# Optimization experiments

Measured on AMD Instinct MI355X. Metric: run time of the kernel, lower is better.

Reference implementation:

```python
import jax, jax.numpy as jnp
import numpy as np
import math

B, TH, STEPS = 4, 120, 8
D_IN, D_MODEL, N_HEADS, N_LAYERS, D_FF = 32, 512, 8, 4, 2048
N_SUB = 5
D_HEAD = D_MODEL // N_HEADS
EPS = 1e-5


def _pos_encoding(T, d):
    pos = jnp.arange(T, dtype=jnp.float32)[:, None]
    div = jnp.exp(jnp.arange(0, d, 2, dtype=jnp.float32) * (-math.log(10000.0) / d))
    pe = jnp.zeros((T, d), dtype=jnp.float32)
    pe = pe.at[:, 0::2].set(jnp.sin(pos * div))
    pe = pe.at[:, 1::2].set(jnp.cos(pos * div))
    return pe


def setup_inputs() -> dict:
    key = jax.random.key(0)
    ks = jax.random.split(key, 16)
    s = 0.02
    n = lambda k, shp: jax.random.normal(k, shp, jnp.float32) * s
    return {
        "history": jax.random.normal(ks[0], (B, TH, D_IN), jnp.float32),
        "steps": STEPS,
        "W_emb": n(ks[1], (D_MODEL, D_IN)),
        "b_emb": jnp.zeros((D_MODEL,), jnp.float32),
        "Wq": n(ks[2], (N_LAYERS, D_MODEL, D_MODEL)),
        "Wk": n(ks[3], (N_LAYERS, D_MODEL, D_MODEL)),
        "Wv": n(ks[4], (N_LAYERS, D_MODEL, D_MODEL)),
        "Wo": n(ks[5], (N_LAYERS, D_MODEL, D_MODEL)),
        "ln1_g": jnp.ones((N_LAYERS, D_MODEL), jnp.float32),
        "ln1_b": jnp.zeros((N_LAYERS, D_MODEL), jnp.float32),
        "W1": n(ks[6], (N_LAYERS, D_FF, D_MODEL)),
        "b1": jnp.zeros((N_LAYERS, D_FF), jnp.float32),
        "W2": n(ks[7], (N_LAYERS, D_MODEL, D_FF)),
        "b2": jnp.zeros((N_LAYERS, D_MODEL), jnp.float32),
        "ln2_g": jnp.ones((N_LAYERS, D_MODEL), jnp.float32),
        "ln2_b": jnp.zeros((N_LAYERS, D_MODEL), jnp.float32),
        "Wr1": n(ks[8], (D_FF, 2 * D_MODEL)),
        "br1": jnp.zeros((D_FF,), jnp.float32),
        "Wr2": n(ks[9], (D_IN, D_FF)),
        "br2": jnp.zeros((D_IN,), jnp.float32),
    }


def _layernorm(x, g, b):
    mu = x.mean(-1, keepdims=True)
    var = ((x - mu) ** 2).mean(-1, keepdims=True)
    return (x - mu) / jnp.sqrt(var + EPS) * g + b


def reference(history, steps, W_emb, b_emb, Wq, Wk, Wv, Wo, ln1_g, ln1_b,
              W1, b1, W2, b2, ln2_g, ln2_b, Wr1, br1, Wr2, br2):
    total_len = TH + steps
    pe = _pos_encoding(total_len, D_MODEL)
    idx = jnp.arange(total_len)
    # NOTE: faithful to source: mask True where kv index > q index (equinox: True = attend)
    mask = idx[:, None] < idx[None, :]
    neg = jnp.finfo(jnp.float32).min
    scale = math.sqrt(D_MODEL)

    def transformer(buf):  # buf: [T, D_IN] -> [T, D_MODEL]
        h = (buf @ W_emb.T + b_emb) * scale + pe
        for l in range(N_LAYERS):
            q = (h @ Wq[l].T).reshape(total_len, N_HEADS, D_HEAD)
            k = (h @ Wk[l].T).reshape(total_len, N_HEADS, D_HEAD)
            v = (h @ Wv[l].T).reshape(total_len, N_HEADS, D_HEAD)
            logits = jnp.einsum("qhd,khd->hqk", q, k) / math.sqrt(D_HEAD)
            logits = jnp.where(mask[None], logits, neg)
            w = jax.nn.softmax(logits, axis=-1)
            attn = jnp.einsum("hqk,khd->qhd", w, v).reshape(total_len, D_MODEL)
            h = _layernorm(h + attn @ Wo[l].T, ln1_g[l], ln1_b[l])
            m = jax.nn.gelu(h @ W1[l].T + b1[l]) @ W2[l].T + b2[l]
            h = _layernorm(h + m, ln2_g[l], ln2_b[l])
        return h

    def refine(start_val, ctx):  # start_val: [D_IN], ctx: [D_MODEL]
        def body(i, cur):
            we = (W_emb @ cur + b_emb) * scale
            comb = jnp.concatenate([we, ctx])
            delta = Wr2 @ jax.nn.gelu(Wr1 @ comb + br1) + br2
            return cur + delta
        return jax.lax.fori_loop(0, N_SUB, body, start_val)

    def single(hist):  # [TH, D_IN] -> [steps, D_IN]
        buf = jnp.zeros((total_len, D_IN), jnp.float32).at[:TH].set(hist)

        def scan_fn(buf, step_idx):
            h = transformer(buf)  # full recompute each decode step (no KV cache)
            ptr = TH + step_idx
            next_val = refine(buf[ptr - 1], h[ptr - 1])
            return buf.at[ptr].set(next_val), next_val

        _, preds = jax.lax.scan(scan_fn, buf, jnp.arange(steps))
        return preds

    return jax.vmap(single)(history)
```

## Files before the change

kernel.cpp:

```cpp
#include <hip/hip_runtime.h>
#include <math.h>

namespace {
constexpr int NB = 4;
constexpr int SEQ = 128;
constexpr int TH_ = 120;
constexpr int NSTEP = 8;
constexpr int DMODEL = 512;
constexpr int NHEAD = 8;
constexpr int DHEAD = 64;
constexpr int DFFN = 2048;
constexpr int DIN = 32;
constexpr int MROWS = NB*SEQ;
constexpr float SCALE_EMB = 22.627416997969522f;
constexpr float LN_EPS = 1e-5f;
constexpr float NEGF = -3.4028234663852886e38f;
constexpr float PE_C = -0.017988946039015984f;
}

using short8 = __attribute__((ext_vector_type(8))) short;
using f32x4  = __attribute__((ext_vector_type(4))) float;

__device__ __forceinline__ float wave_sum(float v){
#pragma unroll
  for(int off=32;off;off>>=1) v += __shfl_xor(v,off,64);
  return v;
}
__device__ __forceinline__ float blk_sum(float v, float* scr){
  v = wave_sum(v);
  __syncthreads();
  if((threadIdx.x&63)==0) scr[threadIdx.x>>6]=v;
  __syncthreads();
  return scr[0]+scr[1]+scr[2]+scr[3];
}
__device__ __forceinline__ float gelu_t(float x){
  float t = 0.7978845608028654f*(x + 0.044715f*x*x*x);
  return 0.5f*x*(1.0f + tanhf(t));
}
__device__ __forceinline__ float pe_val(int t, int d){
  float div = expf((float)(d & ~1) * PE_C);
  float a = (float)t * div;
  return (d & 1) ? cosf(a) : sinf(a);
}
__device__ __forceinline__ unsigned short f2b(float f){
  union { float f; unsigned u; } c; c.f = f;
  unsigned u = c.u + 0x7FFFu + ((c.u>>16)&1u);
  return (unsigned short)(u>>16);
}
__device__ __forceinline__ short8 pack8(const float* f){
  short8 s;
#pragma unroll
  for(int i=0;i<8;i++) s[i] = (short)f2b(f[i]);
  return s;
}

__global__ __launch_bounds__(256) void conv_w(const float* __restrict__ Wq,
                                              const float* __restrict__ Wk,
                                              const float* __restrict__ Wv,
                                              const float* __restrict__ Wo,
                                              const float* __restrict__ W1,
                                              const float* __restrict__ W2,
                                              unsigned short* __restrict__ dst){
  size_t base = ((size_t)blockIdx.x*256 + threadIdx.x)*8;
  if(base >= 12582912u) return;
  const float* src; size_t off;
  if(base < 1048576u){ src=Wq; off=base; }
  else if(base < 2097152u){ src=Wk; off=base-1048576u; }
  else if(base < 3145728u){ src=Wv; off=base-2097152u; }
  else if(base < 4194304u){ src=Wo; off=base-3145728u; }
  else if(base < 8388608u){ src=W1; off=base-4194304u; }
  else { src=W2; off=base-8388608u; }
  float4 a = *(const float4*)(src+off);
  float4 b = *(const float4*)(src+off+4);
  float f[8] = {a.x,a.y,a.z,a.w,b.x,b.y,b.z,b.w};
  *(short8*)(dst + base) = pack8(f);
}

__global__ __launch_bounds__(256) void init_h0(const float* __restrict__ hist,
                                               const float* __restrict__ W_emb,
                                               const float* __restrict__ b_emb,
                                               float* __restrict__ h0,
                                               unsigned short* __restrict__ h0b){
  int bt = blockIdx.x;
  int b = bt >> 7, t = bt & 127;
  __shared__ float x[DIN];
  if(threadIdx.x < DIN)
    x[threadIdx.x] = (t < TH_) ? hist[((size_t)b*TH_ + t)*DIN + threadIdx.x] : 0.f;
  __syncthreads();
  for(int d = threadIdx.x; d < DMODEL; d += 256){
    float s = 0.f;
#pragma unroll 8
    for(int i=0;i<DIN;i++) s += W_emb[d*DIN+i]*x[i];
    float v = SCALE_EMB*(s + b_emb[d]) + pe_val(t,d);
    h0[(size_t)bt*DMODEL + d] = v;
    h0b[(size_t)bt*DMODEL + d] = f2b(v);
  }
}

__global__ __launch_bounds__(256) void init_misc(const float* __restrict__ Wr1,
                                                 const float* __restrict__ W_emb,
                                                 const float* __restrict__ b_emb,
                                                 const float* __restrict__ br1,
                                                 const float* __restrict__ hist,
                                                 float* __restrict__ M1,
                                                 float* __restrict__ cb1,
                                                 float* __restrict__ cur_x){
  __shared__ float row[DMODEL];
  int j0 = blockIdx.x*8;
  for(int jj=0;jj<8;jj++){
    int j = j0+jj;
    for(int k=threadIdx.x;k<DMODEL;k+=256) row[k] = Wr1[(size_t)j*1024 + k];
    __syncthreads();
    if(threadIdx.x < DIN){
      int i = threadIdx.x; float s = 0.f;
      for(int k=0;k<DMODEL;k++) s += row[k]*W_emb[k*DIN+i];
      M1[j*DIN+i] = SCALE_EMB*s;
    } else if(threadIdx.x == DIN){
      float s=0.f;
      for(int k=0;k<DMODEL;k++) s += row[k]*b_emb[k];
      cb1[j] = br1[j] + SCALE_EMB*s;
    }
    __syncthreads();
  }
  if(blockIdx.x==0 && threadIdx.x<NB*DIN){
    int b = threadIdx.x>>5, i = threadIdx.x&31;
    cur_x[b*DIN+i] = hist[((size_t)b*TH_ + (TH_-1))*DIN + i];
  }
}

__global__ __launch_bounds__(256) void lnpass(const float* __restrict__ X,
                                              const float* __restrict__ g,
                                              const float* __restrict__ bta,
                                              float* __restrict__ Y,
                                              unsigned short* __restrict__ Yb){
  int row = blockIdx.x*4 + (threadIdx.x>>6);
  int l = threadIdx.x&63;
  const float* xp = X + (size_t)row*DMODEL + l*8;
  float4 x0 = *(const float4*)xp;
  float4 x1 = *(const float4*)(xp+4);
  float f[8] = {x0.x,x0.y,x0.z,x0.w,x1.x,x1.y,x1.z,x1.w};
  float s = 0.f;
#pragma unroll
  for(int i=0;i<8;i++) s += f[i];
  s = wave_sum(s);
  float mu = s*(1.f/DMODEL);
  float v = 0.f;
#pragma unroll
  for(int i=0;i<8;i++){ float d0=f[i]-mu; v += d0*d0; }
  v = wave_sum(v);
  float rs = rsqrtf(v*(1.f/DMODEL) + LN_EPS);
#pragma unroll
  for(int i=0;i<8;i++){
    int c = l*8+i;
    f[i] = (f[i]-mu)*rs*g[c] + bta[c];
  }
  float* yp = Y + (size_t)row*DMODEL + l*8;
  *(float4*)yp     = make_float4(f[0],f[1],f[2],f[3]);
  *(float4*)(yp+4) = make_float4(f[4],f[5],f[6],f[7]);
  *(short8*)(Yb + (size_t)row*DMODEL + l*8) = pack8(f);
}

__global__ __launch_bounds__(256) void gemm_bf(
    const unsigned short* __restrict__ A16, int Ka,
    const unsigned short* __restrict__ Wa,
    const unsigned short* __restrict__ Wb,
    const unsigned short* __restrict__ Wc,
    const float* __restrict__ bias, const float* __restrict__ resid,
    float* __restrict__ Cf, unsigned short* __restrict__ Cb,
    int c_rs, int c_mode, int act)
{
  int n0 = blockIdx.x*128;
  int m0 = blockIdx.y*64;
  int tid = threadIdx.x, w = tid>>6, ln = tid&63;
  __shared__ __align__(16) unsigned short As[64][72];
  __shared__ __align__(16) unsigned short Bs[128][72];

  const unsigned short* Wsrc; int nrow0;
  if(c_mode==2){ int which = n0>>9; Wsrc = (which==0?Wa:(which==1?Wb:Wc)); nrow0 = n0&511; }
  else { Wsrc = Wa; nrow0 = n0; }

  f32x4 acc[4][2];
#pragma unroll
  for(int i=0;i<4;i++)
#pragma unroll
    for(int j=0;j<2;j++) acc[i][j] = (f32x4){0.f,0.f,0.f,0.f};

  int fr = ln&15, fq = (ln>>4)*8;
  int arow = tid>>2, akq = (tid&3)*16;
  int brow = tid>>1, bkq = (tid&1)*32;

  for(int k0=0;k0<Ka;k0+=64){
    const unsigned short* ap = A16 + (size_t)(m0+arow)*Ka + k0 + akq;
    short8 a0 = *(const short8*)ap;
    short8 a1 = *(const short8*)(ap+8);
    const unsigned short* bp = Wsrc + (size_t)(nrow0+brow)*Ka + k0 + bkq;
    short8 b0 = *(const short8*)bp;
    short8 b1 = *(const short8*)(bp+8);
    short8 b2 = *(const short8*)(bp+16);
    short8 b3 = *(const short8*)(bp+24);
    *(short8*)&As[arow][akq]   = a0;
    *(short8*)&As[arow][akq+8] = a1;
    *(short8*)&Bs[brow][bkq]    = b0;
    *(short8*)&Bs[brow][bkq+8]  = b1;
    *(short8*)&Bs[brow][bkq+16] = b2;
    *(short8*)&Bs[brow][bkq+24] = b3;
    __syncthreads();
    short8 af[4][2], bf[2][2];
#pragma unroll
    for(int kf=0;kf<2;kf++){
#pragma unroll
      for(int rt=0;rt<4;rt++) af[rt][kf] = *(const short8*)&As[rt*16 + fr][kf*32 + fq];
#pragma unroll
      for(int ct=0;ct<2;ct++) bf[ct][kf] = *(const short8*)&Bs[32*w + ct*16 + fr][kf*32 + fq];
    }
#pragma unroll
    for(int kf=0;kf<2;kf++)
#pragma unroll
      for(int rt=0;rt<4;rt++)
#pragma unroll
        for(int ct=0;ct<2;ct++)
          acc[rt][ct] = __builtin_amdgcn_mfma_f32_16x16x32_bf16(af[rt][kf], bf[ct][kf], acc[rt][ct], 0, 0, 0);
    __syncthreads();
  }

#pragma unroll
  for(int rt=0;rt<4;rt++){
#pragma unroll
    for(int ct=0;ct<2;ct++){
      int n = n0 + 32*w + ct*16 + fr;
#pragma unroll
      for(int r=0;r<4;r++){
        int row = m0 + rt*16 + (ln>>4)*4 + r;
        float v = acc[rt][ct][r];
        if(bias)  v += bias[n];
        if(resid) v += resid[(size_t)row*DMODEL + n];
        if(act==1) v = gelu_t(v);
        if(c_mode==0)      Cf[(size_t)row*c_rs + n] = v;
        else if(c_mode==1) Cb[(size_t)row*c_rs + n] = f2b(v);
        else {
          int which = n>>9, rem = n&511;
          int b = row>>7, t = row&127;
          Cf[(size_t)which*(MROWS*DMODEL) +
             ((size_t)(b*NHEAD + (rem>>6))*SEQ + t)*DHEAD + (rem&63)] = v;
        }
      }
    }
  }
}

__global__ __launch_bounds__(256) void attn_k(const float* __restrict__ qb,
                                              const float* __restrict__ kb,
                                              const float* __restrict__ vb,
                                              unsigned short* __restrict__ attb){
  int b = blockIdx.z, h = blockIdx.y;
  int r0 = blockIdx.x*32;
  const float* Kh = kb + (size_t)(b*NHEAD+h)*SEQ*DHEAD;
  const float* Vh = vb + (size_t)(b*NHEAD+h)*SEQ*DHEAD;
  const float* Qh = qb + (size_t)(b*NHEAD+h)*SEQ*DHEAD;
  __shared__ float kv[SEQ][DHEAD];
  __shared__ float wsm[32][132];
  __shared__ float qs[32][68];
  int tid = threadIdx.x;
  int d = tid&63, rr = tid>>6;

  for(int k=rr;k<SEQ;k+=4) kv[k][d ^ (k&60)] = Kh[k*DHEAD + d];
  for(int r=rr;r<32;r+=4)  qs[r][d] = Qh[(size_t)(r0+r)*DHEAD + d];
  __syncthreads();

  {
    int rp = tid>>4;
    int kg = tid&15;
    float acc[2][8];
#pragma unroll
    for(int i=0;i<2;i++)
#pragma unroll
      for(int kk=0;kk<8;kk++) acc[i][kk]=0.f;
#pragma unroll 4
    for(int d4=0;d4<16;d4++){
      float4 q0 = *(const float4*)&qs[2*rp][d4*4];
      float4 q1 = *(const float4*)&qs[2*rp+1][d4*4];
#pragma unroll
      for(int kk=0;kk<8;kk++){
        int k = 8*kg + kk;
        int off = (d4*4) ^ (k&60);
        float4 kv4 = *(const float4*)&kv[k][off];
        acc[0][kk] += q0.x*kv4.x + q0.y*kv4.y + q0.z*kv4.z + q0.w*kv4.w;
        acc[1][kk] += q1.x*kv4.x + q1.y*kv4.y + q1.z*kv4.z + q1.w*kv4.w;
      }
    }
#pragma unroll
    for(int i=0;i<2;i++){
      int t = r0 + 2*rp + i;
#pragma unroll
      for(int kk=0;kk<8;kk++){
        int k = 8*kg + kk;
        wsm[2*rp+i][k] = (k > t) ? acc[i][kk]*0.125f : NEGF;
      }
    }
  }
  __syncthreads();

  {
    int l2 = tid&63, wv = tid>>6;
    for(int r=wv;r<32;r+=4){
      float l0 = wsm[r][l2], l1 = wsm[r][l2+64];
      float m = fmaxf(l0,l1);
#pragma unroll
      for(int off=32;off;off>>=1) m = fmaxf(m, __shfl_xor(m,off,64));
      float e0 = expf(l0-m), e1 = expf(l1-m);
      float s = e0+e1;
      s = wave_sum(s);
      float inv = 1.f/s;
      wsm[r][l2] = e0*inv; wsm[r][l2+64] = e1*inv;
    }
  }
  __syncthreads();

  for(int k=rr;k<SEQ;k+=4) kv[k][d] = Vh[k*DHEAD + d];
  __syncthreads();

  {
    int dq = (tid&15)*4, rg = tid>>4;
    for(int r=rg;r<32;r+=16){
      float4 acc2 = make_float4(0.f,0.f,0.f,0.f);
      for(int k=0;k<SEQ;k++){
        float w0 = wsm[r][k];
        float4 v = *(const float4*)&kv[k][dq];
        acc2.x += w0*v.x; acc2.y += w0*v.y; acc2.z += w0*v.z; acc2.w += w0*v.w;
      }
      int row = b*SEQ + r0 + r;
      unsigned short* op = attb + (size_t)row*DMODEL + h*DHEAD + dq;
      op[0]=f2b(acc2.x); op[1]=f2b(acc2.y); op[2]=f2b(acc2.z); op[3]=f2b(acc2.w);
    }
  }
}

__global__ __launch_bounds__(256) void ctx_k(const float* __restrict__ r2,
                                             const float* __restrict__ g2,
                                             const float* __restrict__ b2,
                                             const float* __restrict__ Wr1,
                                             const float* __restrict__ cb1,
                                             float* __restrict__ ctxt, int ptr){
  int b = blockIdx.y; int j0 = blockIdx.x*128;
  __shared__ float raw[DMODEL], ctx[DMODEL], scr[4];
  int tid = threadIdx.x;
  const float* rp = r2 + (size_t)(b*SEQ + ptr-1)*DMODEL;
  for(int k=tid;k<DMODEL;k+=256) raw[k]=rp[k];
  __syncthreads();
  float s = 0.f;
  for(int k=tid;k<DMODEL;k+=256) s += raw[k];
  s = blk_sum(s, scr);
  float mu = s/(float)DMODEL;
  float v = 0.f;
  for(int k=tid;k<DMODEL;k+=256){ float d0 = raw[k]-mu; v += d0*d0; }
  v = blk_sum(v, scr);
  float rs = rsqrtf(v/(float)DMODEL + LN_EPS);
  for(int k=tid;k<DMODEL;k+=256) ctx[k] = (raw[k]-mu)*rs*g2[k] + b2[k];
  __syncthreads();
  int wv = tid>>6, l2 = tid&63;
  for(int jj=wv;jj<128;jj+=4){
    int j = j0+jj;
    const float* wp = Wr1 + (size_t)j*1024 + 512;
    float acc = 0.f;
#pragma unroll
    for(int q=0;q<8;q++){ int k = l2 + 64*q; acc += wp[k]*ctx[k]; }
    acc = wave_sum(acc);
    if(l2==0) ctxt[b*DFFN + j] = acc + cb1[j];
  }
}

__global__ __launch_bounds__(256) void refine_fin(const float* __restrict__ M1,
                                                  const float* __restrict__ ctxt,
                                                  const float* __restrict__ Wr2,
                                                  const float* __restrict__ br2,
                                                  float* __restrict__ cur_x,
                                                  const float* __restrict__ W_emb,
                                                  const float* __restrict__ b_emb,
                                                  float* __restrict__ out,
                                                  float* __restrict__ h0,
                                                  unsigned short* __restrict__ h0b,
                                                  int s, int ptr){
  int b = blockIdx.x, tid = threadIdx.x;
  __shared__ float cur[DIN], gs[DFFN], dscr[DIN];
  if(tid < DIN) cur[tid] = cur_x[b*DIN + tid];
  __syncthreads();
  for(int sub=0; sub<5; sub++){
    for(int jj=tid; jj<DFFN; jj+=256){
      float u = ctxt[b*DFFN + jj];
      const float* mp = M1 + (size_t)jj*DIN;
#pragma unroll
      for(int p=0;p<8;p++){
        float4 mv = *(const float4*)(mp + 4*p);
        u += mv.x*cur[4*p] + mv.y*cur[4*p+1] + mv.z*cur[4*p+2] + mv.w*cur[4*p+3];
      }
      gs[jj] = gelu_t(u);
    }
    __syncthreads();
    int w = tid>>6, l = tid&63;
#pragma unroll
    for(int q=0;q<8;q++){
      int i = w*8 + q;
      const float* wr = Wr2 + (size_t)i*DFFN;
      float a = 0.f;
#pragma unroll
      for(int p=0;p<8;p++){
        int j0 = p*256 + l*4;
        float4 wv = *(const float4*)(wr + j0);
        float4 gv = *(const float4*)&gs[j0];
        a += wv.x*gv.x + wv.y*gv.y + wv.z*gv.z + wv.w*gv.w;
      }
      a = wave_sum(a);
      if(l==0) dscr[i] = a;
    }
    __syncthreads();
    if(tid < DIN) cur[tid] += dscr[tid] + br2[tid];
    __syncthreads();
  }
  if(tid < DIN){
    out[(b*NSTEP + s)*DIN + tid] = cur[tid];
    cur_x[b*DIN + tid] = cur[tid];
  }
  __syncthreads();
  for(int d=tid; d<DMODEL; d+=256){
    float s2 = 0.f;
#pragma unroll 8
    for(int i=0;i<DIN;i++) s2 += W_emb[d*DIN+i]*cur[i];
    float v = SCALE_EMB*(s2 + b_emb[d]) + pe_val(ptr, d);
    size_t idx = (size_t)(b*SEQ + ptr)*DMODEL + d;
    h0[idx] = v;
    h0b[idx] = f2b(v);
  }
}

extern "C" void kernel_launch(void* const* d_in, const int* in_sizes, int n_in,
                              void* d_out, int out_size, void* d_ws, size_t ws_size,
                              hipStream_t stream) {
  (void)in_sizes; (void)n_in; (void)out_size; (void)ws_size;
  const float* hist = (const float*)d_in[0];
  const float* W_emb= (const float*)d_in[2];
  const float* b_emb= (const float*)d_in[3];
  const float* Wq   = (const float*)d_in[4];
  const float* Wk   = (const float*)d_in[5];
  const float* Wv   = (const float*)d_in[6];
  const float* Wo   = (const float*)d_in[7];
  const float* ln1g = (const float*)d_in[8];
  const float* ln1b = (const float*)d_in[9];
  const float* W1   = (const float*)d_in[10];
  const float* b1   = (const float*)d_in[11];
  const float* W2   = (const float*)d_in[12];
  const float* b2v  = (const float*)d_in[13];
  const float* ln2g = (const float*)d_in[14];
  const float* ln2b = (const float*)d_in[15];
  const float* Wr1  = (const float*)d_in[16];
  const float* br1  = (const float*)d_in[17];
  const float* Wr2  = (const float*)d_in[18];
  const float* br2  = (const float*)d_in[19];
  float* out = (float*)d_out;
  float* ws  = (float*)d_ws;

  const size_t BTD = (size_t)MROWS*DMODEL;
  const size_t BTDH = BTD/2;
  float* h0   = ws;
  unsigned short* h0b = (unsigned short*)(h0 + BTD);
  float* r2   = h0 + BTD + BTDH;
  float* hln  = r2 + BTD;
  float* hp   = hln + BTD;
  unsigned short* hpb = (unsigned short*)(hp + BTD);
  float* qb   = hp + BTD + BTDH;
  float* kb   = qb + BTD;
  float* vb   = kb + BTD;
  unsigned short* attb = (unsigned short*)(vb + BTD);
  unsigned short* hlnb = (unsigned short*)(vb + BTD + BTDH);
  unsigned short* fbuf16 = (unsigned short*)qb;
  float* r1   = qb;
  unsigned short* W16 = (unsigned short*)(qb + 4*BTD);
  float* after_w = qb + 4*BTD + 6291456;
  float* M1   = after_w;
  float* cb1  = M1 + (size_t)DFFN*DIN;
  float* ctxt = cb1 + DFFN;
  float* cur_x= ctxt + NB*DFFN;

  unsigned short* Wq16 = W16;
  unsigned short* Wk16 = W16 + 1048576;
  unsigned short* Wv16 = W16 + 2097152;
  unsigned short* Wo16 = W16 + 3145728;
  unsigned short* W116 = W16 + 4194304;
  unsigned short* W216 = W16 + 8388608;

  conv_w<<<dim3(6144),dim3(256),0,stream>>>(Wq,Wk,Wv,Wo,W1,W2,W16);
  init_h0<<<dim3(MROWS),dim3(256),0,stream>>>(hist,W_emb,b_emb,h0,h0b);
  init_misc<<<dim3(256),dim3(256),0,stream>>>(Wr1,W_emb,b_emb,br1,hist,M1,cb1,cur_x);

  for(int s=0;s<NSTEP;s++){
    int ptr = TH_ + s;
    for(int l=0;l<4;l++){
      if(l>0)
        lnpass<<<dim3(128),dim3(256),0,stream>>>(r2, ln2g+(l-1)*DMODEL, ln2b+(l-1)*DMODEL, hln, hlnb);
      const unsigned short* A16 = (l==0)? h0b : hlnb;
      const float* res1 = (l==0)? h0 : hln;

      gemm_bf<<<dim3(12,8),dim3(256),0,stream>>>(A16, DMODEL,
          Wq16 + (size_t)l*262144, Wk16 + (size_t)l*262144, Wv16 + (size_t)l*262144,
          nullptr, nullptr, qb, nullptr, 0, 2, 0);

      attn_k<<<dim3(4,NHEAD,NB),dim3(256),0,stream>>>(qb,kb,vb,attb);

      gemm_bf<<<dim3(4,8),dim3(256),0,stream>>>(attb, DMODEL,
          Wo16 + (size_t)l*262144, nullptr, nullptr,
          nullptr, res1, r1, nullptr, DMODEL, 0, 0);

      lnpass<<<dim3(128),dim3(256),0,stream>>>(r1, ln1g+l*DMODEL, ln1b+l*DMODEL, hp, hpb);

      gemm_bf<<<dim3(16,8),dim3(256),0,stream>>>(hpb, DMODEL,
          W116 + (size_t)l*1048576, nullptr, nullptr,
          b1 + l*DFFN, nullptr, nullptr, fbuf16, DFFN, 1, 1);

      gemm_bf<<<dim3(4,8),dim3(256),0,stream>>>(fbuf16, DFFN,
          W216 + (size_t)l*1048576, nullptr, nullptr,
          b2v + l*DMODEL, hp, r2, nullptr, DMODEL, 0, 0);
    }

    ctx_k<<<dim3(16,NB),dim3(256),0,stream>>>(r2, ln2g + 3*DMODEL, ln2b + 3*DMODEL,
                                              Wr1, cb1, ctxt, ptr);
    refine_fin<<<dim3(NB),dim3(256),0,stream>>>(M1, ctxt, Wr2, br2, cur_x,
                                                W_emb, b_emb, out, h0, h0b, s, ptr);
  }
}
```

Baseline: 4.746 ms.

## Fuse decode loop into persistent megakernel with grid barriers and fused layernorm

Replaces the roughly 200 per-step kernel launches with one persistent kernel of 256 workgroups that walks through all decode steps and layers, separating stages with an atomic grid-wide barrier. The layernorm passes are folded into the following GEMM's A-tile load, with per-row statistics computed per tile and the fp32 normalized output written only by the first column tile. GEMM tiles shrink to 32 rows so more tiles exist to spread across the workgroups. The aim is to remove launch overhead and the separate layernorm round trips through memory. In exchange it relies on all 256 workgroups being co-resident for the spin barrier to be safe, and every column tile recomputes the row statistics.

```diff
diff --git a/kernel.cpp b/kernel.cpp
--- a/kernel.cpp
+++ b/kernel.cpp
@@ -16,6 +16,7 @@
 constexpr float LN_EPS = 1e-5f;
 constexpr float NEGF = -3.4028234663852886e38f;
 constexpr float PE_C = -0.017988946039015984f;
+constexpr int NWG = 256;
 }
 
 using short8 = __attribute__((ext_vector_type(8))) short;
@@ -25,13 +26,6 @@
 #pragma unroll
   for(int off=32;off;off>>=1) v += __shfl_xor(v,off,64);
   return v;
-}
-__device__ __forceinline__ float blk_sum(float v, float* scr){
-  v = wave_sum(v);
-  __syncthreads();
-  if((threadIdx.x&63)==0) scr[threadIdx.x>>6]=v;
-  __syncthreads();
-  return scr[0]+scr[1]+scr[2]+scr[3];
 }
 __device__ __forceinline__ float gelu_t(float x){
   float t = 0.7978845608028654f*(x + 0.044715f*x*x*x);
@@ -52,6 +46,42 @@
 #pragma unroll
   for(int i=0;i<8;i++) s[i] = (short)f2b(f[i]);
   return s;
+}
+
+union SMem {
+  struct {
+    unsigned short As[32][72];
+    unsigned short Bs[128][72];
+    float mu[32], rs[32];
+  } g;
+  struct {
+    float kv[SEQ][DHEAD];
+    float wsm[32][132];
+    float qs[32][68];
+  } a;
+  struct {
+    float raw[DMODEL]; float ctx[DMODEL]; float scr[4];
+  } c;
+  struct {
+    float cur[DIN]; float dscr[DIN]; float gs[DFFN];
+  } r;
+};
+
+__device__ __forceinline__ void gbar(unsigned* cnt, unsigned* gen){
+  __syncthreads();
+  if(threadIdx.x==0){
+    unsigned g = __hip_atomic_load(gen, __ATOMIC_RELAXED, __HIP_MEMORY_SCOPE_AGENT);
+    __threadfence();
+    if(__hip_atomic_fetch_add(cnt, 1u, __ATOMIC_RELAXED, __HIP_MEMORY_SCOPE_AGENT) == NWG-1u){
+      __hip_atomic_store(cnt, 0u, __ATOMIC_RELAXED, __HIP_MEMORY_SCOPE_AGENT);
+      __hip_atomic_fetch_add(gen, 1u, __ATOMIC_RELEASE, __HIP_MEMORY_SCOPE_AGENT);
+    } else {
+      while(__hip_atomic_load(gen, __ATOMIC_RELAXED, __HIP_MEMORY_SCOPE_AGENT) == g)
+        __builtin_amdgcn_s_sleep(2);
+    }
+    __threadfence();
+  }
+  __syncthreads();
 }
 
 __global__ __launch_bounds__(256) void conv_w(const float* __restrict__ Wq,
@@ -128,261 +158,254 @@
   }
 }
 
-__global__ __launch_bounds__(256) void lnpass(const float* __restrict__ X,
-                                              const float* __restrict__ g,
-                                              const float* __restrict__ bta,
-                                              float* __restrict__ Y,
-                                              unsigned short* __restrict__ Yb){
-  int row = blockIdx.x*4 + (threadIdx.x>>6);
-  int l = threadIdx.x&63;
-  const float* xp = X + (size_t)row*DMODEL + l*8;
-  float4 x0 = *(const float4*)xp;
-  float4 x1 = *(const float4*)(xp+4);
-  float f[8] = {x0.x,x0.y,x0.z,x0.w,x1.x,x1.y,x1.z,x1.w};
-  float s = 0.f;
-#pragma unroll
-  for(int i=0;i<8;i++) s += f[i];
-  s = wave_sum(s);
-  float mu = s*(1.f/DMODEL);
-  float v = 0.f;
-#pragma unroll
-  for(int i=0;i<8;i++){ float d0=f[i]-mu; v += d0*d0; }
-  v = wave_sum(v);
-  float rs = rsqrtf(v*(1.f/DMODEL) + LN_EPS);
-#pragma unroll
-  for(int i=0;i<8;i++){
-    int c = l*8+i;
-    f[i] = (f[i]-mu)*rs*g[c] + bta[c];
-  }
-  float* yp = Y + (size_t)row*DMODEL + l*8;
-  *(float4*)yp     = make_float4(f[0],f[1],f[2],f[3]);
-  *(float4*)(yp+4) = make_float4(f[4],f[5],f[6],f[7]);
-  *(short8*)(Yb + (size_t)row*DMODEL + l*8) = pack8(f);
-}
-
-__global__ __launch_bounds__(256) void gemm_bf(
-    const unsigned short* __restrict__ A16, int Ka,
-    const unsigned short* __restrict__ Wa,
-    const unsigned short* __restrict__ Wb,
-    const unsigned short* __restrict__ Wc,
-    const float* __restrict__ bias, const float* __restrict__ resid,
-    float* __restrict__ Cf, unsigned short* __restrict__ Cb,
-    int c_rs, int c_mode, int act)
+__device__ void gemm_stage(
+    int ntN,
+    const unsigned short* A16,
+    const float* Afp, const float* lng, const float* lnb, float* lnout,
+    int Ka,
+    const unsigned short* W0, const unsigned short* W1w, const unsigned short* W2w,
+    const float* bias, const float* resid,
+    float* Cf, unsigned short* Cb, int c_rs, int cmode, int act,
+    SMem& sm)
 {
-  int n0 = blockIdx.x*128;
-  int m0 = blockIdx.y*64;
-  int tid = threadIdx.x, w = tid>>6, ln = tid&63;
-  __shared__ __align__(16) unsigned short As[64][72];
-  __shared__ __align__(16) unsigned short Bs[128][72];
-
-  const unsigned short* Wsrc; int nrow0;
-  if(c_mode==2){ int which = n0>>9; Wsrc = (which==0?Wa:(which==1?Wb:Wc)); nrow0 = n0&511; }
-  else { Wsrc = Wa; nrow0 = n0; }
-
-  f32x4 acc[4][2];
-#pragma unroll
-  for(int i=0;i<4;i++)
-#pragma unroll
-    for(int j=0;j<2;j++) acc[i][j] = (f32x4){0.f,0.f,0.f,0.f};
-
-  int fr = ln&15, fq = (ln>>4)*8;
-  int arow = tid>>2, akq = (tid&3)*16;
-  int brow = tid>>1, bkq = (tid&1)*32;
-
-  for(int k0=0;k0<Ka;k0+=64){
-    const unsigned short* ap = A16 + (size_t)(m0+arow)*Ka + k0 + akq;
-    short8 a0 = *(const short8*)ap;
-    short8 a1 = *(const short8*)(ap+8);
-    const unsigned short* bp = Wsrc + (size_t)(nrow0+brow)*Ka + k0 + bkq;
-    short8 b0 = *(const short8*)bp;
-    short8 b1 = *(const short8*)(bp+8);
-    short8 b2 = *(const short8*)(bp+16);
-    short8 b3 = *(const short8*)(bp+24);
-    *(short8*)&As[arow][akq]   = a0;
-    *(short8*)&As[arow][akq+8] = a1;
-    *(short8*)&Bs[brow][bkq]    = b0;
-    *(short8*)&Bs[brow][bkq+8]  = b1;
-    *(short8*)&Bs[brow][bkq+16] = b2;
-    *(short8*)&Bs[brow][bkq+24] = b3;
-    __syncthreads();
-    short8 af[4][2], bf[2][2];
-#pragma unroll
-    for(int kf=0;kf<2;kf++){
-#pragma unroll
-      for(int rt=0;rt<4;rt++) af[rt][kf] = *(const short8*)&As[rt*16 + fr][kf*32 + fq];
-#pragma unroll
-      for(int ct=0;ct<2;ct++) bf[ct][kf] = *(const short8*)&Bs[32*w + ct*16 + fr][kf*32 + fq];
-    }
-#pragma unroll
-    for(int kf=0;kf<2;kf++)
-#pragma unroll
-      for(int rt=0;rt<4;rt++)
-#pragma unroll
-        for(int ct=0;ct<2;ct++)
-          acc[rt][ct] = __builtin_amdgcn_mfma_f32_16x16x32_bf16(af[rt][kf], bf[ct][kf], acc[rt][ct], 0, 0, 0);
-    __syncthreads();
-  }
-
-#pragma unroll
-  for(int rt=0;rt<4;rt++){
-#pragma unroll
-    for(int ct=0;ct<2;ct++){
-      int n = n0 + 32*w + ct*16 + fr;
-#pragma unroll
-      for(int r=0;r<4;r++){
-        int row = m0 + rt*16 + (ln>>4)*4 + r;
-        float v = acc[rt][ct][r];
-        if(bias)  v += bias[n];
-        if(resid) v += resid[(size_t)row*DMODEL + n];
-        if(act==1) v = gelu_t(v);
-        if(c_mode==0)      Cf[(size_t)row*c_rs + n] = v;
-        else if(c_mode==1) Cb[(size_t)row*c_rs + n] = f2b(v);
-        else {
-          int which = n>>9, rem = n&511;
-          int b = row>>7, t = row&127;
-          Cf[(size_t)which*(MROWS*DMODEL) +
-             ((size_t)(b*NHEAD + (rem>>6))*SEQ + t)*DHEAD + (rem&63)] = v;
+  int tid = threadIdx.x, w = tid>>6, l = tid&63;
+  int ntiles = 16*ntN;
+  int fr = l&15, fq = (l>>4)*8;
+  int ar = tid>>3, akq = (tid&7)*8;
+  int br_ = tid>>1, bkq = (tid&1)*32;
+
+  for(int tile=blockIdx.x; tile<ntiles; tile+=NWG){
+    int mt = tile/ntN, nt = tile - mt*ntN;
+    int m0 = mt*32, n0 = nt*128;
+    const unsigned short* Wsrc; int nr0;
+    if(cmode==2){ int which = n0>>9; Wsrc = (which==0?W0:(which==1?W1w:W2w)); nr0 = n0&511; }
+    else { Wsrc = W0; nr0 = n0; }
+
+    if(Afp){
+      for(int r8=0;r8<8;r8++){
+        int r = w*8 + r8;
+        const float* ap = Afp + (size_t)(m0+r)*Ka + l*8;
+        float4 x0 = *(const float4*)ap, x1 = *(const float4*)(ap+4);
+        float s = x0.x+x0.y+x0.z+x0.w+x1.x+x1.y+x1.z+x1.w;
+        s = wave_sum(s);
+        float mu = s*(1.f/DMODEL);
+        float v = (x0.x-mu)*(x0.x-mu)+(x0.y-mu)*(x0.y-mu)+(x0.z-mu)*(x0.z-mu)+(x0.w-mu)*(x0.w-mu)
+                + (x1.x-mu)*(x1.x-mu)+(x1.y-mu)*(x1.y-mu)+(x1.z-mu)*(x1.z-mu)+(x1.w-mu)*(x1.w-mu);
+        v = wave_sum(v);
+        float rs = rsqrtf(v*(1.f/DMODEL) + LN_EPS);
+        if(l==0){ sm.g.mu[r]=mu; sm.g.rs[r]=rs; }
+      }
+      __syncthreads();
+    }
+
+    f32x4 acc[2][2];
+#pragma unroll
+    for(int i=0;i<2;i++)
+#pragma unroll
+      for(int j=0;j<2;j++) acc[i][j] = (f32x4){0.f,0.f,0.f,0.f};
+
+    for(int k0=0;k0<Ka;k0+=64){
+      if(A16){
+        *(short8*)&sm.g.As[ar][akq] = *(const short8*)(A16 + (size_t)(m0+ar)*Ka + k0 + akq);
+      } else {
+        const float* ap = Afp + (size_t)(m0+ar)*Ka + k0 + akq;
+        float4 v0 = *(const float4*)ap, v1 = *(const float4*)(ap+4);
+        float f[8] = {v0.x,v0.y,v0.z,v0.w,v1.x,v1.y,v1.z,v1.w};
+        float mu = sm.g.mu[ar], rs = sm.g.rs[ar];
+        int kb = k0 + akq;
+#pragma unroll
+        for(int i=0;i<8;i++) f[i] = (f[i]-mu)*rs*lng[kb+i] + lnb[kb+i];
+        if(lnout && nt==0){
+          float* dp = lnout + (size_t)(m0+ar)*DMODEL + kb;
+          *(float4*)dp     = make_float4(f[0],f[1],f[2],f[3]);
+          *(float4*)(dp+4) = make_float4(f[4],f[5],f[6],f[7]);
         }
-      }
-    }
-  }
-}
-
-__global__ __launch_bounds__(256) void attn_k(const float* __restrict__ qb,
-                                              const float* __restrict__ kb,
-                                              const float* __restrict__ vb,
-                                              unsigned short* __restrict__ attb){
-  int b = blockIdx.z, h = blockIdx.y;
-  int r0 = blockIdx.x*32;
-  const float* Kh = kb + (size_t)(b*NHEAD+h)*SEQ*DHEAD;
-  const float* Vh = vb + (size_t)(b*NHEAD+h)*SEQ*DHEAD;
-  const float* Qh = qb + (size_t)(b*NHEAD+h)*SEQ*DHEAD;
-  __shared__ float kv[SEQ][DHEAD];
-  __shared__ float wsm[32][132];
-  __shared__ float qs[32][68];
+        *(short8*)&sm.g.As[ar][akq] = pack8(f);
+      }
+      {
+        const unsigned short* wp = Wsrc + (size_t)(nr0+br_)*Ka + k0 + bkq;
+        *(short8*)&sm.g.Bs[br_][bkq]    = *(const short8*)wp;
+        *(short8*)&sm.g.Bs[br_][bkq+8]  = *(const short8*)(wp+8);
+        *(short8*)&sm.g.Bs[br_][bkq+16] = *(const short8*)(wp+16);
+        *(short8*)&sm.g.Bs[br_][bkq+24] = *(const short8*)(wp+24);
+      }
+      __syncthreads();
+      short8 af[2][2], bf[2][2];
+#pragma unroll
+      for(int kf=0;kf<2;kf++){
+#pragma unroll
+        for(int rt=0;rt<2;rt++) af[rt][kf] = *(const short8*)&sm.g.As[rt*16 + fr][kf*32 + fq];
+#pragma unroll
+        for(int ct=0;ct<2;ct++) bf[ct][kf] = *(const short8*)&sm.g.Bs[32*w + ct*16 + fr][kf*32 + fq];
+      }
+#pragma unroll
+      for(int kf=0;kf<2;kf++)
+#pragma unroll
+        for(int rt=0;rt<2;rt++)
+#pragma unroll
+          for(int ct=0;ct<2;ct++)
+            acc[rt][ct] = __builtin_amdgcn_mfma_f32_16x16x32_bf16(af[rt][kf], bf[ct][kf], acc[rt][ct], 0, 0, 0);
+      __syncthreads();
+    }
+
+#pragma unroll
+    for(int rt=0;rt<2;rt++){
+#pragma unroll
+      for(int ct=0;ct<2;ct++){
+        int n = n0 + 32*w + ct*16 + fr;
+#pragma unroll
+        for(int r=0;r<4;r++){
+          int row = m0 + rt*16 + (l>>4)*4 + r;
+          float v = acc[rt][ct][r];
+          if(bias)  v += bias[n];
+          if(resid) v += resid[(size_t)row*DMODEL + n];
+          if(act==1) v = gelu_t(v);
+          if(cmode==0)      Cf[(size_t)row*c_rs + n] = v;
+          else if(cmode==1) Cb[(size_t)row*c_rs + n] = f2b(v);
+          else {
+            int which = n>>9, rem = n&511;
+            int b = row>>7, t = row&127;
+            Cf[(size_t)which*(MROWS*DMODEL) +
+               ((size_t)(b*NHEAD + (rem>>6))*SEQ + t)*DHEAD + (rem&63)] = v;
+          }
+        }
+      }
+    }
+  }
+}
+
+__device__ void attn_stage(const float* qb, const float* kb, const float* vb,
+                           unsigned short* attb, SMem& sm){
   int tid = threadIdx.x;
   int d = tid&63, rr = tid>>6;
-
-  for(int k=rr;k<SEQ;k+=4) kv[k][d ^ (k&60)] = Kh[k*DHEAD + d];
-  for(int r=rr;r<32;r+=4)  qs[r][d] = Qh[(size_t)(r0+r)*DHEAD + d];
-  __syncthreads();
-
-  {
-    int rp = tid>>4;
-    int kg = tid&15;
-    float acc[2][8];
-#pragma unroll
-    for(int i=0;i<2;i++)
-#pragma unroll
-      for(int kk=0;kk<8;kk++) acc[i][kk]=0.f;
+  for(int tile=blockIdx.x; tile<128; tile+=NWG){
+    int b = tile>>5, h = (tile>>2)&7, r0 = (tile&3)*32;
+    const float* Kh = kb + (size_t)(b*NHEAD+h)*SEQ*DHEAD;
+    const float* Vh = vb + (size_t)(b*NHEAD+h)*SEQ*DHEAD;
+    const float* Qh = qb + (size_t)(b*NHEAD+h)*SEQ*DHEAD;
+
+    for(int k=rr;k<SEQ;k+=4) sm.a.kv[k][d ^ (k&60)] = Kh[k*DHEAD + d];
+    for(int r=rr;r<32;r+=4)  sm.a.qs[r][d] = Qh[(size_t)(r0+r)*DHEAD + d];
+    __syncthreads();
+
+    {
+      int rp = tid>>4, kg = tid&15;
+      float acc[2][8];
+#pragma unroll
+      for(int i=0;i<2;i++)
+#pragma unroll
+        for(int kk=0;kk<8;kk++) acc[i][kk]=0.f;
 #pragma unroll 4
-    for(int d4=0;d4<16;d4++){
-      float4 q0 = *(const float4*)&qs[2*rp][d4*4];
-      float4 q1 = *(const float4*)&qs[2*rp+1][d4*4];
-#pragma unroll
-      for(int kk=0;kk<8;kk++){
-        int k = 8*kg + kk;
-        int off = (d4*4) ^ (k&60);
-        float4 kv4 = *(const float4*)&kv[k][off];
-        acc[0][kk] += q0.x*kv4.x + q0.y*kv4.y + q0.z*kv4.z + q0.w*kv4.w;
-        acc[1][kk] += q1.x*kv4.x + q1.y*kv4.y + q1.z*kv4.z + q1.w*kv4.w;
-      }
-    }
-#pragma unroll
-    for(int i=0;i<2;i++){
-      int t = r0 + 2*rp + i;
-#pragma unroll
-      for(int kk=0;kk<8;kk++){
-        int k = 8*kg + kk;
-        wsm[2*rp+i][k] = (k > t) ? acc[i][kk]*0.125f : NEGF;
-      }
-    }
-  }
-  __syncthreads();
-
-  {
-    int l2 = tid&63, wv = tid>>6;
-    for(int r=wv;r<32;r+=4){
-      float l0 = wsm[r][l2], l1 = wsm[r][l2+64];
-      float m = fmaxf(l0,l1);
-#pragma unroll
-      for(int off=32;off;off>>=1) m = fmaxf(m, __shfl_xor(m,off,64));
-      float e0 = expf(l0-m), e1 = expf(l1-m);
-      float s = e0+e1;
-      s = wave_sum(s);
-      float inv = 1.f/s;
-      wsm[r][l2] = e0*inv; wsm[r][l2+64] = e1*inv;
-    }
-  }
-  __syncthreads();
-
-  for(int k=rr;k<SEQ;k+=4) kv[k][d] = Vh[k*DHEAD + d];
-  __syncthreads();
-
-  {
-    int dq = (tid&15)*4, rg = tid>>4;
-    for(int r=rg;r<32;r+=16){
-      float4 acc2 = make_float4(0.f,0.f,0.f,0.f);
-      for(int k=0;k<SEQ;k++){
-        float w0 = wsm[r][k];
-        float4 v = *(const float4*)&kv[k][dq];
-        acc2.x += w0*v.x; acc2.y += w0*v.y; acc2.z += w0*v.z; acc2.w += w0*v.w;
-      }
-      int row = b*SEQ + r0 + r;
-      unsigned short* op = attb + (size_t)row*DMODEL + h*DHEAD + dq;
-      op[0]=f2b(acc2.x); op[1]=f2b(acc2.y); op[2]=f2b(acc2.z); op[3]=f2b(acc2.w);
-    }
-  }
-}
-
-__global__ __launch_bounds__(256) void ctx_k(const float* __restrict__ r2,
-                                             const float* __restrict__ g2,
-                                             const float* __restrict__ b2,
-                                             const float* __restrict__ Wr1,
-                                             const float* __restrict__ cb1,
-                                             float* __restrict__ ctxt, int ptr){
-  int b = blockIdx.y; int j0 = blockIdx.x*128;
-  __shared__ float raw[DMODEL], ctx[DMODEL], scr[4];
+      for(int d4=0;d4<16;d4++){
+        float4 q0 = *(const float4*)&sm.a.qs[2*rp][d4*4];
+        float4 q1 = *(const float4*)&sm.a.qs[2*rp+1][d4*4];
+#pragma unroll
+        for(int kk=0;kk<8;kk++){
+          int k = 8*kg + kk;
+          int off = (d4*4) ^ (k&60);
+          float4 kv4 = *(const float4*)&sm.a.kv[k][off];
+          acc[0][kk] += q0.x*kv4.x + q0.y*kv4.y + q0.z*kv4.z + q0.w*kv4.w;
+          acc[1][kk] += q1.x*kv4.x + q1.y*kv4.y + q1.z*kv4.z + q1.w*kv4.w;
+        }
+      }
+#pragma unroll
+      for(int i=0;i<2;i++){
+        int t = r0 + 2*rp + i;
+#pragma unroll
+        for(int kk=0;kk<8;kk++){
+          int k = 8*kg + kk;
+          sm.a.wsm[2*rp+i][k] = (k > t) ? acc[i][kk]*0.125f : NEGF;
+        }
+      }
+    }
+    __syncthreads();
+
+    {
+      int l2 = tid&63, wv = tid>>6;
+      for(int r=wv;r<32;r+=4){
+        float l0 = sm.a.wsm[r][l2], l1 = sm.a.wsm[r][l2+64];
+        float m = fmaxf(l0,l1);
+#pragma unroll
+        for(int off=32;off;off>>=1) m = fmaxf(m, __shfl_xor(m,off,64));
+        float e0 = expf(l0-m), e1 = expf(l1-m);
+        float s = e0+e1;
+        s = wave_sum(s);
+        float inv = 1.f/s;
+        sm.a.wsm[r][l2] = e0*inv; sm.a.wsm[r][l2+64] = e1*inv;
+      }
+    }
+    __syncthreads();
+
+    for(int k=rr;k<SEQ;k+=4) sm.a.kv[k][d] = Vh[k*DHEAD + d];
+    __syncthreads();
+
+    {
+      int dq = (tid&15)*4, rg = tid>>4;
+      for(int r=rg;r<32;r+=16){
+        float4 a2 = make_float4(0.f,0.f,0.f,0.f);
+        for(int k=0;k<SEQ;k++){
+          float w0 = sm.a.wsm[r][k];
+          float4 v = *(const float4*)&sm.a.kv[k][dq];
+          a2.x += w0*v.x; a2.y += w0*v.y; a2.z += w0*v.z; a2.w += w0*v.w;
+        }
+        int row = b*SEQ + r0 + r;
+        unsigned short* op = attb + (size_t)row*DMODEL + h*DHEAD + dq;
+        op[0]=f2b(a2.x); op[1]=f2b(a2.y); op[2]=f2b(a2.z); op[3]=f2b(a2.w);
+      }
+    }
+    __syncthreads();
+  }
+}
+
+__device__ float blk_sum(float v, float* scr){
+  v = wave_sum(v);
+  __syncthreads();
+  if((threadIdx.x&63)==0) scr[threadIdx.x>>6]=v;
+  __syncthreads();
+  return scr[0]+scr[1]+scr[2]+scr[3];
+}
+
+__device__ void ctx_stage(const float* r2, const float* g2, const float* b2,
+                          const float* Wr1, const float* cb1,
+                          float* ctxt, int ptr, SMem& sm){
   int tid = threadIdx.x;
-  const float* rp = r2 + (size_t)(b*SEQ + ptr-1)*DMODEL;
-  for(int k=tid;k<DMODEL;k+=256) raw[k]=rp[k];
-  __syncthreads();
-  float s = 0.f;
-  for(int k=tid;k<DMODEL;k+=256) s += raw[k];
-  s = blk_sum(s, scr);
-  float mu = s/(float)DMODEL;
-  float v = 0.f;
-  for(int k=tid;k<DMODEL;k+=256){ float d0 = raw[k]-mu; v += d0*d0; }
-  v = blk_sum(v, scr);
-  float rs = rsqrtf(v/(float)DMODEL + LN_EPS);
-  for(int k=tid;k<DMODEL;k+=256) ctx[k] = (raw[k]-mu)*rs*g2[k] + b2[k];
-  __syncthreads();
-  int wv = tid>>6, l2 = tid&63;
-  for(int jj=wv;jj<128;jj+=4){
-    int j = j0+jj;
-    const float* wp = Wr1 + (size_t)j*1024 + 512;
-    float acc = 0.f;
-#pragma unroll
-    for(int q=0;q<8;q++){ int k = l2 + 64*q; acc += wp[k]*ctx[k]; }
-    acc = wave_sum(acc);
-    if(l2==0) ctxt[b*DFFN + j] = acc + cb1[j];
-  }
-}
-
-__global__ __launch_bounds__(256) void refine_fin(const float* __restrict__ M1,
-                                                  const float* __restrict__ ctxt,
-                                                  const float* __restrict__ Wr2,
-                                                  const float* __restrict__ br2,
-                                                  float* __restrict__ cur_x,
-                                                  const float* __restrict__ W_emb,
-                                                  const float* __restrict__ b_emb,
-                                                  float* __restrict__ out,
-                                                  float* __restrict__ h0,
-                                                  unsigned short* __restrict__ h0b,
-                                                  int s, int ptr){
+  for(int tile=blockIdx.x; tile<64; tile+=NWG){
+    int b = tile>>4, j0 = (tile&15)*128;
+    const float* rp = r2 + (size_t)(b*SEQ + ptr-1)*DMODEL;
+    for(int k=tid;k<DMODEL;k+=256) sm.c.raw[k]=rp[k];
+    __syncthreads();
+    float s = 0.f;
+    for(int k=tid;k<DMODEL;k+=256) s += sm.c.raw[k];
+    s = blk_sum(s, sm.c.scr);
+    float mu = s/(float)DMODEL;
+    float v = 0.f;
+    for(int k=tid;k<DMODEL;k+=256){ float d0 = sm.c.raw[k]-mu; v += d0*d0; }
+    v = blk_sum(v, sm.c.scr);
+    float rs = rsqrtf(v/(float)DMODEL + LN_EPS);
+    for(int k=tid;k<DMODEL;k+=256) sm.c.ctx[k] = (sm.c.raw[k]-mu)*rs*g2[k] + b2[k];
+    __syncthreads();
+    int wv = tid>>6, l2 = tid&63;
+    for(int jj=wv;jj<128;jj+=4){
+      int j = j0+jj;
+      const float* wp = Wr1 + (size_t)j*1024 + 512;
+      float acc = 0.f;
+#pragma unroll
+      for(int q=0;q<8;q++){ int k = l2 + 64*q; acc += wp[k]*sm.c.ctx[k]; }
+      acc = wave_sum(acc);
+      if(l2==0) ctxt[b*DFFN + j] = acc + cb1[j];
+    }
+    __syncthreads();
+  }
+}
+
+__device__ void refine_stage(const float* M1, const float* ctxt,
+                             const float* Wr2, const float* br2,
+                             float* cur_x, const float* W_emb, const float* b_emb,
+                             float* out, float* h0, unsigned short* h0b,
+                             int s, int ptr, SMem& sm){
+  if(blockIdx.x >= NB) return;
   int b = blockIdx.x, tid = threadIdx.x;
-  __shared__ float cur[DIN], gs[DFFN], dscr[DIN];
-  if(tid < DIN) cur[tid] = cur_x[b*DIN + tid];
+  if(tid < DIN) sm.r.cur[tid] = cur_x[b*DIN + tid];
   __syncthreads();
   for(int sub=0; sub<5; sub++){
     for(int jj=tid; jj<DFFN; jj+=256){
@@ -391,9 +414,9 @@
 #pragma unroll
       for(int p=0;p<8;p++){
         float4 mv = *(const float4*)(mp + 4*p);
-        u += mv.x*cur[4*p] + mv.y*cur[4*p+1] + mv.z*cur[4*p+2] + mv.w*cur[4*p+3];
-      }
-      gs[jj] = gelu_t(u);
+        u += mv.x*sm.r.cur[4*p] + mv.y*sm.r.cur[4*p+1] + mv.z*sm.r.cur[4*p+2] + mv.w*sm.r.cur[4*p+3];
+      }
+      sm.r.gs[jj] = gelu_t(u);
     }
     __syncthreads();
     int w = tid>>6, l = tid&63;
@@ -406,29 +429,96 @@
       for(int p=0;p<8;p++){
         int j0 = p*256 + l*4;
         float4 wv = *(const float4*)(wr + j0);
-        float4 gv = *(const float4*)&gs[j0];
+        float4 gv = *(const float4*)&sm.r.gs[j0];
         a += wv.x*gv.x + wv.y*gv.y + wv.z*gv.z + wv.w*gv.w;
       }
       a = wave_sum(a);
-      if(l==0) dscr[i] = a;
-    }
-    __syncthreads();
-    if(tid < DIN) cur[tid] += dscr[tid] + br2[tid];
+      if(l==0) sm.r.dscr[i] = a;
+    }
+    __syncthreads();
+    if(tid < DIN) sm.r.cur[tid] += sm.r.dscr[tid] + br2[tid];
     __syncthreads();
   }
   if(tid < DIN){
-    out[(b*NSTEP + s)*DIN + tid] = cur[tid];
-    cur_x[b*DIN + tid] = cur[tid];
+    out[(b*NSTEP + s)*DIN + tid] = sm.r.cur[tid];
+    cur_x[b*DIN + tid] = sm.r.cur[tid];
   }
   __syncthreads();
   for(int d=tid; d<DMODEL; d+=256){
     float s2 = 0.f;
 #pragma unroll 8
-    for(int i=0;i<DIN;i++) s2 += W_emb[d*DIN+i]*cur[i];
+    for(int i=0;i<DIN;i++) s2 += W_emb[d*DIN+i]*sm.r.cur[i];
     float v = SCALE_EMB*(s2 + b_emb[d]) + pe_val(ptr, d);
     size_t idx = (size_t)(b*SEQ + ptr)*DMODEL + d;
     h0[idx] = v;
     h0b[idx] = f2b(v);
+  }
+}
+
+__global__ __launch_bounds__(256) void mega(
+    const float* __restrict__ ln1g, const float* __restrict__ ln1b,
+    const float* __restrict__ ln2g, const float* __restrict__ ln2b,
+    const float* __restrict__ b1, const float* __restrict__ b2v,
+    const float* __restrict__ Wr1, const float* __restrict__ Wr2,
+    const float* __restrict__ br2,
+    const float* __restrict__ W_emb, const float* __restrict__ b_emb,
+    const float* cb1, const float* M1, float* cur_x,
+    float* h0, unsigned short* h0b, float* r2, float* hln,
+    float* qb, unsigned short* attb, unsigned short* fb16,
+    const unsigned short* W16, float* ctxt, float* out,
+    unsigned* bar)
+{
+  __shared__ SMem sm;
+  unsigned* cnt = bar;
+  unsigned* gen = bar + 32;
+  float* r1 = qb;
+  float* hp = qb + 2*(size_t)MROWS*DMODEL;
+  const size_t BTD = (size_t)MROWS*DMODEL;
+
+#pragma unroll 1
+  for(int s=0;s<NSTEP;s++){
+    int ptr = TH_ + s;
+#pragma unroll 1
+    for(int l=0;l<4;l++){
+      const unsigned short* Wq16 = W16 + (size_t)l*262144;
+      const unsigned short* Wk16 = W16 + 1048576 + (size_t)l*262144;
+      const unsigned short* Wv16 = W16 + 2097152 + (size_t)l*262144;
+      const unsigned short* Wo16 = W16 + 3145728 + (size_t)l*262144;
+      const unsigned short* W116 = W16 + 4194304 + (size_t)l*1048576;
+      const unsigned short* W216 = W16 + 8388608 + (size_t)l*1048576;
+
+      if(l==0)
+        gemm_stage(12, h0b, nullptr,nullptr,nullptr,nullptr, DMODEL,
+                   Wq16,Wk16,Wv16, nullptr,nullptr, qb,nullptr, 0, 2, 0, sm);
+      else
+        gemm_stage(12, nullptr, r2, ln2g+(l-1)*DMODEL, ln2b+(l-1)*DMODEL, hln, DMODEL,
+                   Wq16,Wk16,Wv16, nullptr,nullptr, qb,nullptr, 0, 2, 0, sm);
+      gbar(cnt,gen);
+
+      attn_stage(qb, qb+BTD, qb+2*BTD, attb, sm);
+      gbar(cnt,gen);
+
+      gemm_stage(4, attb, nullptr,nullptr,nullptr,nullptr, DMODEL,
+                 Wo16,nullptr,nullptr, nullptr, (l==0)?h0:hln,
+                 r1,nullptr, DMODEL, 0, 0, sm);
+      gbar(cnt,gen);
+
+      gemm_stage(16, nullptr, r1, ln1g+l*DMODEL, ln1b+l*DMODEL, hp, DMODEL,
+                 W116,nullptr,nullptr, b1+l*DFFN, nullptr,
+                 nullptr, fb16, DFFN, 1, 1, sm);
+      gbar(cnt,gen);
+
+      gemm_stage(4, fb16, nullptr,nullptr,nullptr,nullptr, DFFN,
+                 W216,nullptr,nullptr, b2v+l*DMODEL, hp,
+                 r2,nullptr, DMODEL, 0, 0, sm);
+      gbar(cnt,gen);
+    }
+
+    ctx_stage(r2, ln2g+3*DMODEL, ln2b+3*DMODEL, Wr1, cb1, ctxt, ptr, sm);
+    gbar(cnt,gen);
+
+    refine_stage(M1, ctxt, Wr2, br2, cur_x, W_emb, b_emb, out, h0, h0b, s, ptr, sm);
+    gbar(cnt,gen);
   }
 }
 
@@ -459,70 +549,28 @@
   float* ws  = (float*)d_ws;
 
   const size_t BTD = (size_t)MROWS*DMODEL;
-  const size_t BTDH = BTD/2;
-  float* h0   = ws;
-  unsigned short* h0b = (unsigned short*)(h0 + BTD);
-  float* r2   = h0 + BTD + BTDH;
-  float* hln  = r2 + BTD;
-  float* hp   = hln + BTD;
-  unsigned short* hpb = (unsigned short*)(hp + BTD);
-  float* qb   = hp + BTD + BTDH;
-  float* kb   = qb + BTD;
-  float* vb   = kb + BTD;
-  unsigned short* attb = (unsigned short*)(vb + BTD);
-  unsigned short* hlnb = (unsigned short*)(vb + BTD + BTDH);
-  unsigned short* fbuf16 = (unsigned short*)qb;
-  float* r1   = qb;
-  unsigned short* W16 = (unsigned short*)(qb + 4*BTD);
-  float* after_w = qb + 4*BTD + 6291456;
-  float* M1   = after_w;
-  float* cb1  = M1 + (size_t)DFFN*DIN;
-  float* ctxt = cb1 + DFFN;
-  float* cur_x= ctxt + NB*DFFN;
-
-  unsigned short* Wq16 = W16;
-  unsigned short* Wk16 = W16 + 1048576;
-  unsigned short* Wv16 = W16 + 2097152;
-  unsigned short* Wo16 = W16 + 3145728;
-  unsigned short* W116 = W16 + 4194304;
-  unsigned short* W216 = W16 + 8388608;
-
+
+  unsigned* bar = (unsigned*)ws;
+  float* p = ws + 64;
+  float* h0 = p;                      p += BTD;
+  unsigned short* h0b = (unsigned short*)p; p += BTD/2;
+  float* r2 = p;                      p += BTD;
+  float* hln = p;                     p += BTD;
+  float* qb = p;                      p += 3*BTD;
+  unsigned short* attb = (unsigned short*)p; p += BTD/2;
+  unsigned short* fb16 = (unsigned short*)p; p += 2*BTD;
+  unsigned short* W16 = (unsigned short*)p;  p += 6291456;
+  float* M1 = p;                      p += (size_t)DFFN*DIN;
+  float* cb1 = p;                     p += DFFN;
+  float* ctxt = p;                    p += NB*DFFN;
+  float* cur_x = p;                   p += NB*DIN;
+
+  hipMemsetAsync(bar, 0, 256, stream);
   conv_w<<<dim3(6144),dim3(256),0,stream>>>(Wq,Wk,Wv,Wo,W1,W2,W16);
   init_h0<<<dim3(MROWS),dim3(256),0,stream>>>(hist,W_emb,b_emb,h0,h0b);
   init_misc<<<dim3(256),dim3(256),0,stream>>>(Wr1,W_emb,b_emb,br1,hist,M1,cb1,cur_x);
 
-  for(int s=0;s<NSTEP;s++){
-    int ptr = TH_ + s;
-    for(int l=0;l<4;l++){
-      if(l>0)
-        lnpass<<<dim3(128),dim3(256),0,stream>>>(r2, ln2g+(l-1)*DMODEL, ln2b+(l-1)*DMODEL, hln, hlnb);
-      const unsigned short* A16 = (l==0)? h0b : hlnb;
-      const float* res1 = (l==0)? h0 : hln;
-
-      gemm_bf<<<dim3(12,8),dim3(256),0,stream>>>(A16, DMODEL,
-          Wq16 + (size_t)l*262144, Wk16 + (size_t)l*262144, Wv16 + (size_t)l*262144,
-          nullptr, nullptr, qb, nullptr, 0, 2, 0);
-
-      attn_k<<<dim3(4,NHEAD,NB),dim3(256),0,stream>>>(qb,kb,vb,attb);
-
-      gemm_bf<<<dim3(4,8),dim3(256),0,stream>>>(attb, DMODEL,
-          Wo16 + (size_t)l*262144, nullptr, nullptr,
-          nullptr, res1, r1, nullptr, DMODEL, 0, 0);
-
-      lnpass<<<dim3(128),dim3(256),0,stream>>>(r1, ln1g+l*DMODEL, ln1b+l*DMODEL, hp, hpb);
-
-      gemm_bf<<<dim3(16,8),dim3(256),0,stream>>>(hpb, DMODEL,
-          W116 + (size_t)l*1048576, nullptr, nullptr,
-          b1 + l*DFFN, nullptr, nullptr, fbuf16, DFFN, 1, 1);
-
-      gemm_bf<<<dim3(4,8),dim3(256),0,stream>>>(fbuf16, DFFN,
-          W216 + (size_t)l*1048576, nullptr, nullptr,
-          b2v + l*DMODEL, hp, r2, nullptr, DMODEL, 0, 0);
-    }
-
-    ctx_k<<<dim3(16,NB),dim3(256),0,stream>>>(r2, ln2g + 3*DMODEL, ln2b + 3*DMODEL,
-                                              Wr1, cb1, ctxt, ptr);
-    refine_fin<<<dim3(NB),dim3(256),0,stream>>>(M1, ctxt, Wr2, br2, cur_x,
-                                                W_emb, b_emb, out, h0, h0b, s, ptr);
-  }
-}
+  mega<<<dim3(NWG),dim3(256),0,stream>>>(
+      ln1g,ln1b,ln2g,ln2b,b1,b2v,Wr1,Wr2,br2,W_emb,b_emb,
+      cb1,M1,cur_x,h0,h0b,r2,hln,qb,attb,fb16,W16,ctxt,out,bar);
+}
```

Result: slower. 6.180 ms (+30.2%).
